# Kernel tuning notes

Measured on AMD Instinct MI355X. Metric: run time of the kernel, lower is better.

## Reference

```python
import jax, jax.numpy as jnp
import numpy as np

N, M, D = 8192, 8192, 64
_LIM = 36.0

def _softplus(x):
    # LogexpTransformation.inverse_transform: x if x > 36 else log1p(exp(x))
    return jnp.where(x > _LIM, x, jnp.log1p(jnp.exp(jnp.minimum(x, _LIM))))

def setup_inputs() -> dict:
    key = jax.random.key(0)
    k1, k2, k3 = jax.random.split(key, 3)
    X = jax.random.normal(k1, (N, D), dtype=jnp.float32)
    Z = jax.random.normal(k2, (M, D), dtype=jnp.float32)
    l_raw = jax.random.uniform(k3, (D,), dtype=jnp.float32)
    sigma_f_raw = jnp.ones((), dtype=jnp.float32)
    return {"X": X, "Z": Z, "l_raw": l_raw, "sigma_f_raw": sigma_f_raw}

def reference(X, Z, l_raw, sigma_f_raw):
    l = _softplus(l_raw)                     # [D] length scales
    sigma_f = _softplus(sigma_f_raw)         # scalar signal variance
    inv_length = 1.0 / (l * l)               # [D]
    w = jnp.sqrt(inv_length)                 # scale features instead of [N,M,D] broadcast
    Xs = X * w                               # [N,D]
    Zs = Z * w                               # [M,D]
    # sum_d inv_length[d]*(X-Z)^2 = |Xs|^2 + |Zs|^2 - 2 Xs.Zs  (GEMM-expansion)
    x2 = jnp.sum(Xs * Xs, axis=1)            # [N]
    z2 = jnp.sum(Zs * Zs, axis=1)            # [M]
    cross = Xs @ Zs.T                        # [N,M]
    dist = x2[:, None] + z2[None, :] - 2.0 * cross
    return sigma_f * jnp.exp(-0.5 * dist)
```

## Files before the change

### kernel.cpp

```cpp
#include <hip/hip_runtime.h>
#include <hip/hip_bf16.h>
#include <math.h>

#define NROWS 8192
#define MCOLS 8192
#define DK    64

typedef _Float16 f16x8 __attribute__((ext_vector_type(8)));
typedef __attribute__((ext_vector_type(8))) short bf16x8;
typedef __attribute__((ext_vector_type(4))) float f32x4;

#define WS_XH 0u
#define WS_ZH (1u << 20)
#define WS_HX (2u << 20)
#define WS_HZ ((2u << 20) + 32768u)
#define WS_NEED ((size_t)(2u << 20) + 65536u)

#define SQRT_L2E 1.2011224087864498f

__device__ __forceinline__ float softplus_f(float x) {
    return x > 36.0f ? x : log1pf(expf(fminf(x, 36.0f)));
}

__global__ void rbf_prep(const float* __restrict__ X, const float* __restrict__ Z,
                         const float* __restrict__ lraw, const float* __restrict__ sraw,
                         char* __restrict__ ws) {
    __shared__ float wsc[DK];
    if (threadIdx.x < DK)
        wsc[threadIdx.x] = SQRT_L2E / softplus_f(lraw[threadIdx.x]);
    __syncthreads();

    int tid = blockIdx.x * 256 + threadIdx.x;
    bool isZ = tid >= 65536;
    int t = tid & 65535;
    int row = t >> 3;
    int kc = t & 7;
    const float* src = (isZ ? Z : X) + (size_t)row * DK + kc * 8;
    float4 v0 = *(const float4*)(src);
    float4 v1 = *(const float4*)(src + 4);
    float f[8] = {v0.x, v0.y, v0.z, v0.w, v1.x, v1.y, v1.z, v1.w};
    f16x8 hv;
    float sq = 0.0f;
    #pragma unroll
    for (int j = 0; j < 8; ++j) {
        _Float16 h = (_Float16)(f[j] * wsc[kc * 8 + j]);
        hv[j] = h;
        float hf = (float)h;
        sq += hf * hf;
    }
    sq += __shfl_xor(sq, 1);
    sq += __shfl_xor(sq, 2);
    sq += __shfl_xor(sq, 4);
    *(f16x8*)(ws + (isZ ? WS_ZH : WS_XH) + (size_t)row * 128 + kc * 16) = hv;
    if (kc == 0) {
        float* nrm = (float*)(ws + (isZ ? WS_HZ : WS_HX));
        float v = 0.5f * sq;
        if (isZ) v -= log2f(softplus_f(sraw[0]));
        nrm[row] = v;
    }
}

__launch_bounds__(512, 4)
__global__ void rbf_main(const char* __restrict__ ws, float* __restrict__ out) {
    __shared__ __align__(16) char smem[32768];

    int bid = blockIdx.x;
    int s = (bid & 7) * 512 + (bid >> 3);
    int tR = s >> 6, tC = s & 63;

    const int tid = threadIdx.x;

    #pragma unroll
    for (int c = 0; c < 4; ++c) {
        int o = c * 8192 + tid * 16;
        bool isB = o >= 16384;
        int oo = o & 16383;
        int row = oo >> 7;
        int colb = oo & 127;
        const char* src = ws + (isB ? WS_ZH : WS_XH)
                        + (size_t)((isB ? tC : tR) * 128 + row) * 128 + colb;
        float4 v = *(const float4*)(src);
        int dst = (isB ? 16384 : 0) + row * 128 + (colb ^ ((row & 7) << 4));
        *(float4*)(smem + dst) = v;
    }
    __syncthreads();

    const int lane = tid & 63;
    const int wid  = tid >> 6;
    const int wr = wid >> 1;
    const int wc = wid & 1;
    const int lr = lane & 15;
    const int lg = lane >> 4;
    const int swz = (lr & 7) << 4;

    f32x4 acc[2][4];
    #pragma unroll
    for (int a = 0; a < 2; ++a)
        #pragma unroll
        for (int b = 0; b < 4; ++b) acc[a][b] = f32x4{0.f, 0.f, 0.f, 0.f};

    #pragma unroll
    for (int ks = 0; ks < 2; ++ks) {
        int kb = ((lg * 16 + ks * 64) ^ swz);
        f16x8 af[2], bfr[4];
        #pragma unroll
        for (int mi = 0; mi < 2; ++mi)
            af[mi] = *(const f16x8*)(smem + (wr * 32 + mi * 16 + lr) * 128 + kb);
        #pragma unroll
        for (int ni = 0; ni < 4; ++ni)
            bfr[ni] = *(const f16x8*)(smem + 16384 + (wc * 64 + ni * 16 + lr) * 128 + kb);
        #pragma unroll
        for (int mi = 0; mi < 2; ++mi)
            #pragma unroll
            for (int ni = 0; ni < 4; ++ni)
                acc[mi][ni] = __builtin_amdgcn_mfma_f32_16x16x32_f16(
                    bfr[ni], af[mi], acc[mi][ni], 0, 0, 0);
    }

    const float* hx = (const float*)(ws + WS_HX);
    const float* hz = (const float*)(ws + WS_HZ);
    #pragma unroll
    for (int mi = 0; mi < 2; ++mi) {
        int xrow = tR * 128 + wr * 32 + mi * 16 + lr;
        float hxv = hx[xrow];
        size_t rbase = (size_t)xrow * MCOLS;
        #pragma unroll
        for (int ni = 0; ni < 4; ++ni) {
            int zc0 = tC * 128 + wc * 64 + ni * 16 + lg * 4;
            float4 hzv = *(const float4*)(hz + zc0);
            float4 o;
            o.x = __builtin_amdgcn_exp2f(acc[mi][ni][0] - hxv - hzv.x);
            o.y = __builtin_amdgcn_exp2f(acc[mi][ni][1] - hxv - hzv.y);
            o.z = __builtin_amdgcn_exp2f(acc[mi][ni][2] - hxv - hzv.z);
            o.w = __builtin_amdgcn_exp2f(acc[mi][ni][3] - hxv - hzv.w);
            *(float4*)(out + rbase + zc0) = o;
        }
    }
}

__launch_bounds__(512, 4)
__global__ void rbf_fused(const float* __restrict__ X, const float* __restrict__ Z,
                          const float* __restrict__ lraw, const float* __restrict__ sraw,
                          float* __restrict__ out) {
    __shared__ __align__(16) char smem[65536];
    __shared__ float hxz[256];
    __shared__ float wsc[DK];
    __shared__ float sigf_s;

    const int tid = threadIdx.x;
    const int tR = blockIdx.y;
    const int tC = blockIdx.x;

    if (tid < DK) wsc[tid] = 1.0f / softplus_f(lraw[tid]);
    if (tid == 511) sigf_s = softplus_f(sraw[0]);
    __syncthreads();

    #pragma unroll
    for (int i = 0; i < 4; ++i) {
        int rfull = i * 64 + (tid >> 3);
        int r = rfull & 127;
        int kc = tid & 7;
        bool isB = rfull >= 128;
        const float* src = isB ? (Z + (size_t)(tC * 128 + r) * DK + kc * 8)
                               : (X + (size_t)(tR * 128 + r) * DK + kc * 8);
        float4 v0 = *(const float4*)(src);
        float4 v1 = *(const float4*)(src + 4);
        float f[8] = {v0.x, v0.y, v0.z, v0.w, v1.x, v1.y, v1.z, v1.w};
        bf16x8 hv, lv;
        float sq = 0.0f;
        #pragma unroll
        for (int j = 0; j < 8; ++j) {
            float fv = f[j] * wsc[kc * 8 + j];
            sq += fv * fv;
            unsigned int u = __float_as_uint(fv);
            u += 0x7fffu + ((u >> 16) & 1u);
            unsigned short h = (unsigned short)(u >> 16);
            hv[j] = (short)h;
            float hf = __uint_as_float(((unsigned int)h) << 16);
            unsigned int u2 = __float_as_uint(fv - hf);
            u2 += 0x7fffu + ((u2 >> 16) & 1u);
            lv[j] = (short)(unsigned short)(u2 >> 16);
        }
        sq += __shfl_xor(sq, 1);
        sq += __shfl_xor(sq, 2);
        sq += __shfl_xor(sq, 4);
        if (kc == 0) hxz[rfull] = 0.5f * sq;
        int halfOff = isB ? 32768 : 0;
        int byteOff = r * 128 + ((kc * 16) ^ ((r & 7) << 4));
        *(bf16x8*)(smem + halfOff + byteOff) = hv;
        *(bf16x8*)(smem + halfOff + 16384 + byteOff) = lv;
    }
    __syncthreads();

    const int lane = tid & 63;
    const int wid  = tid >> 6;
    const int wr = wid >> 1;
    const int wc = wid & 1;
    const int lr = lane & 15;
    const int lg = lane >> 4;
    const int swz = (lr & 7) << 4;

    f32x4 acc[2][4];
    #pragma unroll
    for (int a = 0; a < 2; ++a)
        #pragma unroll
        for (int b = 0; b < 4; ++b) acc[a][b] = f32x4{0.f, 0.f, 0.f, 0.f};

    #pragma unroll
    for (int pass = 0; pass < 3; ++pass) {
        const char* Ap = smem + ((pass == 2) ? 16384 : 0);
        const char* Bp = smem + 32768 + ((pass == 1) ? 16384 : 0);
        #pragma unroll
        for (int ks = 0; ks < 2; ++ks) {
            int kb = ((lg * 16 + ks * 64) ^ swz);
            bf16x8 af[2], bfr[4];
            #pragma unroll
            for (int mi = 0; mi < 2; ++mi)
                af[mi] = *(const bf16x8*)(Ap + (wr * 32 + mi * 16 + lr) * 128 + kb);
            #pragma unroll
            for (int ni = 0; ni < 4; ++ni)
                bfr[ni] = *(const bf16x8*)(Bp + (wc * 64 + ni * 16 + lr) * 128 + kb);
            #pragma unroll
            for (int mi = 0; mi < 2; ++mi)
                #pragma unroll
                for (int ni = 0; ni < 4; ++ni)
                    acc[mi][ni] = __builtin_amdgcn_mfma_f32_16x16x32_bf16(
                        af[mi], bfr[ni], acc[mi][ni], 0, 0, 0);
        }
    }

    const float sf = sigf_s;
    #pragma unroll
    for (int mi = 0; mi < 2; ++mi) {
        int row0 = wr * 32 + mi * 16 + lg * 4;
        #pragma unroll
        for (int ni = 0; ni < 4; ++ni) {
            int col = wc * 64 + ni * 16 + lr;
            float hzv = hxz[128 + col];
            size_t obase = (size_t)(tR * 128 + row0) * MCOLS + (size_t)(tC * 128 + col);
            #pragma unroll
            for (int j = 0; j < 4; ++j) {
                float arg = acc[mi][ni][j] - (hxz[row0 + j] + hzv);
                out[obase + (size_t)j * MCOLS] = sf * __expf(arg);
            }
        }
    }
}

extern "C" void kernel_launch(void* const* d_in, const int* in_sizes, int n_in,
                              void* d_out, int out_size, void* d_ws, size_t ws_size,
                              hipStream_t stream) {
    const float* X = (const float*)d_in[0];
    const float* Z = (const float*)d_in[1];
    const float* l = (const float*)d_in[2];
    const float* s = (const float*)d_in[3];
    float* out = (float*)d_out;
    if (ws_size >= WS_NEED && d_ws != nullptr) {
        char* ws = (char*)d_ws;
        rbf_prep<<<512, 256, 0, stream>>>(X, Z, l, s, ws);
        rbf_main<<<4096, 512, 0, stream>>>(ws, out);
    } else {
        dim3 grid(MCOLS / 128, NROWS / 128);
        rbf_fused<<<grid, dim3(512), 0, stream>>>(X, Z, l, s, out);
    }
}
```

Before: 63.78 us.

## Persist blocks over column tiles with double-buffered Z staging in rbf_main

Each block now keeps its X tile in registers and loops over 8 consecutive column tiles, double-buffering Z tiles in shared memory and prefetching the next tile into registers while the current tile's MFMA and exp work runs. The grid drops from 4096 to 512 blocks, and the MFMA operand order is swapped so each lane writes scalar column-strided stores instead of float4 row stores. The aim is to remove repeated X loads and per-tile launch and sync overhead and to overlap global loads with compute. The cost is lower parallelism, 512 blocks on a 256-CU device, and possibly less coalesced output stores in a store-bound kernel.

```diff
diff --git a/kernel.cpp b/kernel.cpp
--- a/kernel.cpp
+++ b/kernel.cpp
@@ -5,6 +5,7 @@
 #define NROWS 8192
 #define MCOLS 8192
 #define DK    64
+#define TILE_G 8
 
 typedef _Float16 f16x8 __attribute__((ext_vector_type(8)));
 typedef __attribute__((ext_vector_type(8))) short bf16x8;
@@ -62,78 +63,107 @@
 
 __launch_bounds__(512, 4)
 __global__ void rbf_main(const char* __restrict__ ws, float* __restrict__ out) {
-    __shared__ __align__(16) char smem[32768];
+    __shared__ __align__(16) char smem[49152];
 
     int bid = blockIdx.x;
-    int s = (bid & 7) * 512 + (bid >> 3);
-    int tR = s >> 6, tC = s & 63;
-
-    const int tid = threadIdx.x;
-
-    #pragma unroll
-    for (int c = 0; c < 4; ++c) {
-        int o = c * 8192 + tid * 16;
-        bool isB = o >= 16384;
-        int oo = o & 16383;
-        int row = oo >> 7;
-        int colb = oo & 127;
-        const char* src = ws + (isB ? WS_ZH : WS_XH)
-                        + (size_t)((isB ? tC : tR) * 128 + row) * 128 + colb;
-        float4 v = *(const float4*)(src);
-        int dst = (isB ? 16384 : 0) + row * 128 + (colb ^ ((row & 7) << 4));
-        *(float4*)(smem + dst) = v;
-    }
-    __syncthreads();
-
+    int s = (bid & 7) * 64 + (bid >> 3);
+    int tR = s >> 3;
+    int cg = s & 7;
+
+    const int tid  = threadIdx.x;
     const int lane = tid & 63;
     const int wid  = tid >> 6;
-    const int wr = wid >> 1;
-    const int wc = wid & 1;
-    const int lr = lane & 15;
-    const int lg = lane >> 4;
+    const int wr = wid >> 1, wc = wid & 1;
+    const int lr = lane & 15, lg = lane >> 4;
     const int swz = (lr & 7) << 4;
 
-    f32x4 acc[2][4];
-    #pragma unroll
-    for (int a = 0; a < 2; ++a)
-        #pragma unroll
-        for (int b = 0; b < 4; ++b) acc[a][b] = f32x4{0.f, 0.f, 0.f, 0.f};
-
-    #pragma unroll
-    for (int ks = 0; ks < 2; ++ks) {
-        int kb = ((lg * 16 + ks * 64) ^ swz);
-        f16x8 af[2], bfr[4];
+    const int o0 = tid * 16, o1 = tid * 16 + 8192;
+    const int r0 = o0 >> 7, cb0 = o0 & 127;
+    const int r1 = o1 >> 7, cb1 = o1 & 127;
+    const int d0 = r0 * 128 + (cb0 ^ ((r0 & 7) << 4));
+    const int d1 = r1 * 128 + (cb1 ^ ((r1 & 7) << 4));
+
+    {
+        const char* xsrc = ws + WS_XH + (size_t)tR * 16384;
+        *(float4*)(smem + d0) = *(const float4*)(xsrc + o0);
+        *(float4*)(smem + d1) = *(const float4*)(xsrc + o1);
+        const char* zsrc = ws + WS_ZH + (size_t)(cg * TILE_G) * 16384;
+        *(float4*)(smem + 16384 + d0) = *(const float4*)(zsrc + o0);
+        *(float4*)(smem + 16384 + d1) = *(const float4*)(zsrc + o1);
+    }
+    __syncthreads();
+
+    f16x8 xf[2][2];
+    #pragma unroll
+    for (int ks = 0; ks < 2; ++ks)
         #pragma unroll
         for (int mi = 0; mi < 2; ++mi)
-            af[mi] = *(const f16x8*)(smem + (wr * 32 + mi * 16 + lr) * 128 + kb);
-        #pragma unroll
-        for (int ni = 0; ni < 4; ++ni)
-            bfr[ni] = *(const f16x8*)(smem + 16384 + (wc * 64 + ni * 16 + lr) * 128 + kb);
-        #pragma unroll
-        for (int mi = 0; mi < 2; ++mi)
-            #pragma unroll
-            for (int ni = 0; ni < 4; ++ni)
-                acc[mi][ni] = __builtin_amdgcn_mfma_f32_16x16x32_f16(
-                    bfr[ni], af[mi], acc[mi][ni], 0, 0, 0);
-    }
+            xf[ks][mi] = *(const f16x8*)(smem + (wr * 32 + mi * 16 + lr) * 128
+                                         + ((lg * 16 + ks * 64) ^ swz));
 
     const float* hx = (const float*)(ws + WS_HX);
     const float* hz = (const float*)(ws + WS_HZ);
-    #pragma unroll
-    for (int mi = 0; mi < 2; ++mi) {
-        int xrow = tR * 128 + wr * 32 + mi * 16 + lr;
-        float hxv = hx[xrow];
-        size_t rbase = (size_t)xrow * MCOLS;
-        #pragma unroll
-        for (int ni = 0; ni < 4; ++ni) {
-            int zc0 = tC * 128 + wc * 64 + ni * 16 + lg * 4;
-            float4 hzv = *(const float4*)(hz + zc0);
-            float4 o;
-            o.x = __builtin_amdgcn_exp2f(acc[mi][ni][0] - hxv - hzv.x);
-            o.y = __builtin_amdgcn_exp2f(acc[mi][ni][1] - hxv - hzv.y);
-            o.z = __builtin_amdgcn_exp2f(acc[mi][ni][2] - hxv - hzv.z);
-            o.w = __builtin_amdgcn_exp2f(acc[mi][ni][3] - hxv - hzv.w);
-            *(float4*)(out + rbase + zc0) = o;
+    float4 hxa[2];
+    #pragma unroll
+    for (int mi = 0; mi < 2; ++mi)
+        hxa[mi] = *(const float4*)(hx + tR * 128 + wr * 32 + mi * 16 + lg * 4);
+
+    for (int g = 0; g < TILE_G; ++g) {
+        const int cur = g & 1;
+        const int tC = cg * TILE_G + g;
+
+        float4 z0, z1;
+        if (g + 1 < TILE_G) {
+            const char* zsrc = ws + WS_ZH + (size_t)(tC + 1) * 16384;
+            z0 = *(const float4*)(zsrc + o0);
+            z1 = *(const float4*)(zsrc + o1);
+        }
+
+        const char* zb = smem + 16384 + cur * 16384;
+        f32x4 acc[2][4];
+        #pragma unroll
+        for (int a = 0; a < 2; ++a)
+            #pragma unroll
+            for (int b = 0; b < 4; ++b) acc[a][b] = f32x4{0.f, 0.f, 0.f, 0.f};
+        #pragma unroll
+        for (int ks = 0; ks < 2; ++ks) {
+            const int kb = ((lg * 16 + ks * 64) ^ swz);
+            f16x8 bfr[4];
+            #pragma unroll
+            for (int ni = 0; ni < 4; ++ni)
+                bfr[ni] = *(const f16x8*)(zb + (wc * 64 + ni * 16 + lr) * 128 + kb);
+            #pragma unroll
+            for (int mi = 0; mi < 2; ++mi)
+                #pragma unroll
+                for (int ni = 0; ni < 4; ++ni)
+                    acc[mi][ni] = __builtin_amdgcn_mfma_f32_16x16x32_f16(
+                        xf[ks][mi], bfr[ni], acc[mi][ni], 0, 0, 0);
+        }
+
+        float hzv[4];
+        #pragma unroll
+        for (int ni = 0; ni < 4; ++ni)
+            hzv[ni] = hz[tC * 128 + wc * 64 + ni * 16 + lr];
+        #pragma unroll
+        for (int mi = 0; mi < 2; ++mi) {
+            int grow0 = tR * 128 + wr * 32 + mi * 16 + lg * 4;
+            #pragma unroll
+            for (int ni = 0; ni < 4; ++ni) {
+                int gcol = tC * 128 + wc * 64 + ni * 16 + lr;
+                size_t obase = (size_t)grow0 * MCOLS + gcol;
+                #pragma unroll
+                for (int j = 0; j < 4; ++j) {
+                    float arg = acc[mi][ni][j] - hxa[mi][j] - hzv[ni];
+                    out[obase + (size_t)j * MCOLS] = __builtin_amdgcn_exp2f(arg);
+                }
+            }
+        }
+
+        if (g + 1 < TILE_G) {
+            char* zn = smem + 16384 + (1 - cur) * 16384;
+            *(float4*)(zn + d0) = z0;
+            *(float4*)(zn + d1) = z1;
+            __syncthreads();
         }
     }
 }
@@ -258,7 +288,7 @@
     if (ws_size >= WS_NEED && d_ws != nullptr) {
         char* ws = (char*)d_ws;
         rbf_prep<<<512, 256, 0, stream>>>(X, Z, l, s, ws);
-        rbf_main<<<4096, 512, 0, stream>>>(ws, out);
+        rbf_main<<<512, 512, 0, stream>>>(ws, out);
     } else {
         dim3 grid(MCOLS / 128, NROWS / 128);
         rbf_fused<<<grid, dim3(512), 0, stream>>>(X, Z, l, s, out);
```

Result: faster. 53.37 us (-16.3%).
